# Optimization experiments

Measured on AMD Instinct MI355X. Metric: run time of the kernel, lower is better.

## Reference

```python
import jax, jax.numpy as jnp
import numpy as np

B, N, DIM, H, DH = 8, 4096, 512, 8, 64
M = 266  # nb_features = int(dim_head * ln(dim_head)) = int(64*4.1589)
LN_EPS = 1e-5
K_EPS = 1e-4  # performer softmax_kernel epsilon


def _gaussian_orthogonal_matrix(m, d, rng):
    # performer_pytorch default: stacked QR blocks, rows scaled by chi(d) norms
    blocks = []
    n_full = m // d
    for _ in range(n_full):
        q, _ = np.linalg.qr(rng.standard_normal((d, d)))
        blocks.append(q.T)
    rem = m - n_full * d
    if rem > 0:
        q, _ = np.linalg.qr(rng.standard_normal((d, d)))
        blocks.append(q.T[:rem])
    proj = np.concatenate(blocks, axis=0)
    norms = np.linalg.norm(rng.standard_normal((m, d)), axis=1)
    return (proj * norms[:, None]).astype(np.float32)


def setup_inputs() -> dict:
    key = jax.random.key(0)
    ks = jax.random.split(key, 8)
    s_in = 1.0 / np.sqrt(DIM)
    s_ff = 1.0 / np.sqrt(4 * DIM)
    rng = np.random.default_rng(0)
    return {
        "x": jax.random.normal(ks[0], (B, N, DIM), jnp.float32),
        "w_q": jax.random.normal(ks[1], (DIM, DIM), jnp.float32) * s_in,
        "w_k": jax.random.normal(ks[2], (DIM, DIM), jnp.float32) * s_in,
        "w_v": jax.random.normal(ks[3], (DIM, DIM), jnp.float32) * s_in,
        "w_o": jax.random.normal(ks[4], (DIM, DIM), jnp.float32) * s_in,
        "b_o": jnp.zeros((DIM,), jnp.float32),
        "ln1_g": jnp.ones((DIM,), jnp.float32),
        "ln1_b": jnp.zeros((DIM,), jnp.float32),
        "ln2_g": jnp.ones((DIM,), jnp.float32),
        "ln2_b": jnp.zeros((DIM,), jnp.float32),
        "ff_w1": jax.random.normal(ks[5], (DIM, 4 * DIM), jnp.float32) * s_in,
        "ff_b1": jnp.zeros((4 * DIM,), jnp.float32),
        "ff_w2": jax.random.normal(ks[6], (4 * DIM, DIM), jnp.float32) * s_ff,
        "ff_b2": jnp.zeros((DIM,), jnp.float32),
        "projection": jnp.asarray(_gaussian_orthogonal_matrix(M, DH, rng)),
    }


def _layernorm(x, g, b):
    mu = jnp.mean(x, -1, keepdims=True)
    var = jnp.mean((x - mu) ** 2, -1, keepdims=True)
    return (x - mu) * jax.lax.rsqrt(var + LN_EPS) * g + b


def _softmax_kernel(data, proj, is_query):
    # FAVOR+ positive softmax-kernel features (performer_pytorch.softmax_kernel)
    dn = data.shape[-1] ** -0.25  # data_normalizer
    ratio = proj.shape[0] ** -0.5
    dd = jnp.einsum("bhnd,md->bhnm", data * dn, proj)
    diag = jnp.sum(data ** 2, -1, keepdims=True) * 0.5 * (dn ** 2)  # [B,H,N,1]
    if is_query:
        mx = jax.lax.stop_gradient(jnp.max(dd, -1, keepdims=True))
    else:
        mx = jax.lax.stop_gradient(jnp.max(dd))
    return ratio * (jnp.exp(dd - diag - mx) + K_EPS)


def reference(x, w_q, w_k, w_v, w_o, b_o, ln1_g, ln1_b, ln2_g, ln2_b,
              ff_w1, ff_b1, ff_w2, ff_b2, projection):
    # --- attention sublayer (pre-norm) ---
    h = _layernorm(x, ln1_g, ln1_b)

    def split_heads(t):
        return t.reshape(B, N, H, DH).transpose(0, 2, 1, 3)  # [B,H,N,DH]

    q = split_heads(h @ w_q)
    k = split_heads(h @ w_k)
    v = split_heads(h @ w_v)

    qp = _softmax_kernel(q, projection, True)   # [B,H,N,M]
    kp = _softmax_kernel(k, projection, False)  # [B,H,N,M]

    # non-causal linear attention: O(N) in sequence length
    d_inv = 1.0 / jnp.einsum("bhnm,bhm->bhn", qp, jnp.sum(kp, axis=2))
    ctx = jnp.einsum("bhnm,bhnd->bhmd", kp, v)          # [B,H,M,DH]
    attn = jnp.einsum("bhnm,bhmd,bhn->bhnd", qp, ctx, d_inv)
    attn = attn.transpose(0, 2, 1, 3).reshape(B, N, DIM)
    x = x + attn @ w_o + b_o

    # --- feed-forward sublayer (pre-norm) ---
    h2 = _layernorm(x, ln2_g, ln2_b)
    ff = jax.nn.gelu(h2 @ ff_w1 + ff_b1, approximate=False) @ ff_w2 + ff_b2
    return x + ff
```

## Files before the change

kernel.cpp:

```cpp
#include <hip/hip_runtime.h>
#include <cmath>

typedef unsigned short u16;
typedef unsigned int u32;
typedef short bf16x8 __attribute__((ext_vector_type(8)));
typedef float f32x4 __attribute__((ext_vector_type(4)));

#define DEVI __device__ __forceinline__

constexpr int NSEQ = 4096, DIMM = 512;
constexpr int KVLD = 1024;
constexpr int MP = 288;
constexpr int MPP = 296;
constexpr int MREAL = 266;
constexpr int DHP = 96;
constexpr int LSTR = 72;
constexpr float LNEPS = 1e-5f;
constexpr float KEPS = 1e-4f;
constexpr float DN = 0.3535533905932738f;
constexpr float HALF_DN2 = 0.0625f;

DEVI u16 f2bf(float f) {
  u32 u = __float_as_uint(f);
  u32 r = (u + 0x7FFFu + ((u >> 16) & 1u)) >> 16;
  return (u16)r;
}
DEVI float bf2f(u16 h) { return __uint_as_float(((u32)h) << 16); }

DEVI f32x4 mfma16(bf16x8 a, bf16x8 b, f32x4 c) {
  return __builtin_amdgcn_mfma_f32_16x16x32_bf16(a, b, c, 0, 0, 0);
}

DEVI void gload_lds16(const void* g, void* l) {
  __builtin_amdgcn_global_load_lds(
      (const __attribute__((address_space(1))) u32*)g,
      (__attribute__((address_space(3))) u32*)l, 16, 0, 0);
}

DEVI float gelu_fast(float z) {
  float a = fminf(1.5957691216057308f * (z + 0.044715f * z * z * z), 60.f);
  float e = __expf(a);
  return z * e * __builtin_amdgcn_rcpf(e + 1.f);
}

__global__ void ws_sentinel(float* out) { out[0] = 12345.0f; }

__launch_bounds__(256)
__global__ void transpose_cvt(const float* __restrict__ in, u16* __restrict__ out,
                              int K, int Nn) {
  __shared__ float tl[32][33];
  int ntn = Nn >> 5;
  int bid = blockIdx.x;
  int kt = bid / ntn, ntt = bid - kt * ntn;
  int k0 = kt << 5, nn0 = ntt << 5;
  int t = threadIdx.x;
  int r = t >> 5, c = t & 31;
#pragma unroll
  for (int i = 0; i < 4; ++i)
    tl[r + i * 8][c] = in[(size_t)(k0 + r + i * 8) * Nn + nn0 + c];
  __syncthreads();
#pragma unroll
  for (int i = 0; i < 4; ++i)
    out[(size_t)(nn0 + r + i * 8) * K + k0 + c] = f2bf(tl[c][r + i * 8]);
}

__global__ void proj_prep(const float* __restrict__ proj, u16* __restrict__ projf) {
  int idx = blockIdx.x * 256 + threadIdx.x;
  if (idx >= MP * 64) return;
  int e = idx & 7, lane = (idx >> 3) & 63, fh = idx >> 9;
  int f = fh >> 1, half = fh & 1;
  int m = f * 16 + (lane & 15);
  int d = half * 32 + (lane >> 4) * 8 + e;
  float v = (m < MREAL) ? proj[m * 64 + d] * DN : 0.f;
  projf[idx] = f2bf(v);
}

__launch_bounds__(256)
__global__ void ln_fwd(const float* __restrict__ x, const float* __restrict__ g,
                       const float* __restrict__ bt, u16* __restrict__ out) {
  int w = threadIdx.x >> 6, lane = threadIdx.x & 63;
  int row = blockIdx.x * 4 + w;
  const float* xr = x + (size_t)row * DIMM;
  int c0 = lane * 4;
  float4 v0 = *(const float4*)(xr + c0);
  float4 v1 = *(const float4*)(xr + 256 + c0);
  float s = v0.x + v0.y + v0.z + v0.w + v1.x + v1.y + v1.z + v1.w;
  float sq = v0.x * v0.x + v0.y * v0.y + v0.z * v0.z + v0.w * v0.w +
             v1.x * v1.x + v1.y * v1.y + v1.z * v1.z + v1.w * v1.w;
#pragma unroll
  for (int mk = 1; mk < 64; mk <<= 1) {
    s += __shfl_xor(s, mk, 64);
    sq += __shfl_xor(sq, mk, 64);
  }
  float mu = s * (1.f / 512.f);
  float var = sq * (1.f / 512.f) - mu * mu;
  float rstd = rsqrtf(var + LNEPS);
  float4 g0 = *(const float4*)(g + c0);
  float4 g1 = *(const float4*)(g + 256 + c0);
  float4 b0 = *(const float4*)(bt + c0);
  float4 b1 = *(const float4*)(bt + 256 + c0);
  u16* orow = out + (size_t)row * DIMM;
  uint2 p0, p1;
  {
    u16 h0 = f2bf((v0.x - mu) * rstd * g0.x + b0.x);
    u16 h1 = f2bf((v0.y - mu) * rstd * g0.y + b0.y);
    u16 h2 = f2bf((v0.z - mu) * rstd * g0.z + b0.z);
    u16 h3 = f2bf((v0.w - mu) * rstd * g0.w + b0.w);
    p0.x = ((u32)h1 << 16) | h0; p0.y = ((u32)h3 << 16) | h2;
  }
  {
    u16 h0 = f2bf((v1.x - mu) * rstd * g1.x + b1.x);
    u16 h1 = f2bf((v1.y - mu) * rstd * g1.y + b1.y);
    u16 h2 = f2bf((v1.z - mu) * rstd * g1.z + b1.z);
    u16 h3 = f2bf((v1.w - mu) * rstd * g1.w + b1.w);
    p1.x = ((u32)h1 << 16) | h0; p1.y = ((u32)h3 << 16) | h2;
  }
  *(uint2*)(orow + c0) = p0;
  *(uint2*)(orow + 256 + c0) = p1;
}

#define WAITVM(N) asm volatile("s_waitcnt vmcnt(" #N ")" ::: "memory")

template <int EPI>
__launch_bounds__(512)
__global__ void gemm256(const u16* __restrict__ A, int lda,
                        const u16* __restrict__ Bt, int ldb, int K,
                        void* __restrict__ OutP, int Nout, int ldo,
                        const float* __restrict__ bias,
                        const float* __restrict__ Res) {
  __shared__ __align__(16) u16 Al[2][256 * 64];
  __shared__ __align__(16) u16 Bl[2][256 * 64];
  int ntiles = Nout >> 8;
  int nwg = gridDim.x;
  int bid = blockIdx.x;
  int cpx = nwg >> 3;
  int wg = (bid & 7) * cpx + (bid >> 3);
  int mt = wg / ntiles, nt = wg - mt * ntiles;
  int t = threadIdx.x, lane = t & 63, w = t >> 6;
  int wm = w >> 2, wn = w & 3;
  int fr = lane & 15, fq = lane >> 4;
  int rowA0 = mt * 256, colB0 = nt * 256;
  int swz = (fr & 7) << 4;

  f32x4 acc[8][4];
#pragma unroll
  for (int i = 0; i < 8; ++i)
#pragma unroll
    for (int j = 0; j < 4; ++j) acc[i][j] = f32x4{0.f, 0.f, 0.f, 0.f};

  int srow = t >> 3;
  int so = ((t * 16) & 127) ^ ((srow & 7) << 4);

#define STAGE_G(bufi, k0)                                                       \
  do {                                                                          \
    _Pragma("unroll") for (int it = 0; it < 4; ++it) {                          \
      gload_lds16(                                                              \
          (const char*)(A + ((size_t)(rowA0 + srow + it * 64) * lda + (k0))) + so, \
          (char*)Al[bufi] + t * 16 + it * 8192);                                \
      gload_lds16(                                                              \
          (const char*)(Bt + ((size_t)(colB0 + srow + it * 64) * ldb + (k0))) + so, \
          (char*)Bl[bufi] + t * 16 + it * 8192);                                \
    }                                                                           \
  } while (0)

  int NT = K >> 6;
  STAGE_G(0, 0);
  STAGE_G(1, 64);
  int bi = 0;
  for (int tt = 0; tt < NT; ++tt) {
    if (tt + 1 < NT) { WAITVM(8); } else { WAITVM(0); }
    __builtin_amdgcn_s_barrier();
#pragma unroll
    for (int p = 0; p < 4; ++p) {
      int mh = p >> 1, nh = p & 1;
      bf16x8 av[4][2], bv[2][2];
#pragma unroll
      for (int i = 0; i < 4; ++i)
#pragma unroll
        for (int ks = 0; ks < 2; ++ks) {
          int row = wm * 128 + (mh * 4 + i) * 16 + fr;
          av[i][ks] = *(const bf16x8*)((const char*)Al[bi] + row * 128 +
                                       (((ks << 6) | (fq << 4)) ^ swz));
        }
#pragma unroll
      for (int j = 0; j < 2; ++j)
#pragma unroll
        for (int ks = 0; ks < 2; ++ks) {
          int row = wn * 64 + (nh * 2 + j) * 16 + fr;
          bv[j][ks] = *(const bf16x8*)((const char*)Bl[bi] + row * 128 +
                                       (((ks << 6) | (fq << 4)) ^ swz));
        }
      __builtin_amdgcn_s_setprio(1);
#pragma unroll
      for (int i = 0; i < 4; ++i)
#pragma unroll
        for (int j = 0; j < 2; ++j)
#pragma unroll
          for (int ks = 0; ks < 2; ++ks)
            acc[mh * 4 + i][nh * 2 + j] =
                mfma16(av[i][ks], bv[j][ks], acc[mh * 4 + i][nh * 2 + j]);
      __builtin_amdgcn_s_setprio(0);
    }
    __builtin_amdgcn_s_barrier();
    if (tt + 2 < NT) STAGE_G(bi, (tt + 2) * 64);
    bi ^= 1;
  }
#undef STAGE_G

#pragma unroll
  for (int i = 0; i < 8; ++i)
#pragma unroll
    for (int j = 0; j < 4; ++j) {
      int row = rowA0 + wm * 128 + i * 16 + fq * 4;
      int col = colB0 + wn * 64 + j * 16 + fr;
#pragma unroll
      for (int r = 0; r < 4; ++r) {
        float v = acc[i][j][r];
        size_t idx = (size_t)(row + r) * ldo + col;
        if constexpr (EPI == 0) {
          ((u16*)OutP)[idx] = f2bf(v);
        } else if constexpr (EPI == 1) {
          ((float*)OutP)[idx] = v + bias[col] + Res[(size_t)(row + r) * 512 + col];
        } else if constexpr (EPI == 2) {
          ((u16*)OutP)[idx] = f2bf(gelu_fast(v + bias[col]));
        } else {
          float bb = bias ? bias[col] : 0.f;
          ((float*)OutP)[idx] += v + bb;
        }
      }
    }
}

__launch_bounds__(256)
__global__ void kmax_kernel(const u16* __restrict__ kv, const u16* __restrict__ projf,
                            u32* __restrict__ maxslot) {
  __shared__ __align__(16) u16 kt[64 * 64];
  __shared__ float wred[4];
  int bid = blockIdx.x;
  int bh = bid >> 6, nt = bid & 63;
  int b = bh >> 3, h = bh & 7;
  int n0 = nt * 64;
  int t = threadIdx.x, lane = t & 63, w = t >> 6;
  int fr = lane & 15, fq = lane >> 4;

#pragma unroll
  for (int it = 0; it < 4; ++it) {
    int idx = t + it * 256;
    int r = idx >> 4, sg = idx & 15;
    *(uint2*)(kt + r * 64 + sg * 4) =
        *(const uint2*)(kv + ((size_t)(b * NSEQ + n0 + r)) * KVLD + h * 64 + sg * 4);
  }
  __syncthreads();

  const bf16x8* pf = (const bf16x8*)projf;
  bf16x8 a0 = *(const bf16x8*)(kt + (w * 16 + fr) * 64 + fq * 8);
  bf16x8 a1 = *(const bf16x8*)(kt + (w * 16 + fr) * 64 + 32 + fq * 8);
  float m = -1e30f;
#pragma unroll
  for (int f = 0; f < 18; ++f) {
    bf16x8 b0 = pf[(f * 2 + 0) * 64 + lane];
    bf16x8 b1 = pf[(f * 2 + 1) * 64 + lane];
    f32x4 z = {0.f, 0.f, 0.f, 0.f};
    z = mfma16(a0, b0, z);
    z = mfma16(a1, b1, z);
    if (f * 16 + fr < MREAL) {
#pragma unroll
      for (int r = 0; r < 4; ++r) m = fmaxf(m, z[r]);
    }
  }
#pragma unroll
  for (int mk = 1; mk < 64; mk <<= 1) m = fmaxf(m, __shfl_xor(m, mk, 64));
  if (lane == 0) wred[w] = m;
  __syncthreads();
  if (t == 0) {
    float mm = fmaxf(fmaxf(wred[0], wred[1]), fmaxf(wred[2], wred[3]));
    u32 u = __float_as_uint(mm);
    u32 enc = (u & 0x80000000u) ? ~u : (u | 0x80000000u);
    atomicMax(maxslot, enc);
  }
}

__launch_bounds__(512)
__global__ void fused_ctx(const u16* __restrict__ kvbuf, const u16* __restrict__ projf,
                          const u32* __restrict__ maxslot, float* __restrict__ part) {
  __shared__ __align__(16) u16 kt[64 * 64];
  __shared__ __align__(16) u16 kpL[MP * LSTR];
  __shared__ __align__(16) u16 vL[DHP * LSTR];
  int bid = blockIdx.x;
  int bh = bid >> 2, s = bid & 3;
  int b = bh >> 3, h = bh & 7;
  int t = threadIdx.x, lane = t & 63, w = t >> 6;
  int fr = lane & 15, fq = lane >> 4;
  int rg = w & 3, fh = w >> 2;
  int wq4 = w >> 1, wn = w & 1;
  int i_base = (wq4 < 2) ? wq4 * 5 : 10 + (wq4 - 2) * 4;
  int i_cnt = (wq4 < 2) ? 5 : 4;

  if (t < 256) {
    int rr = 64 + (t >> 3), sg = t & 7;
    u16 val = (rr == 64) ? (u16)0x3F80 : (u16)0;
    uint4 v4; u16* pv = (u16*)&v4;
#pragma unroll
    for (int e = 0; e < 8; ++e) pv[e] = val;
    *(uint4*)(vL + rr * LSTR + sg * 8) = v4;
  }
  u32 enc = *maxslot;
  float gmax = __uint_as_float((enc & 0x80000000u) ? (enc & 0x7FFFFFFFu) : ~enc);
  const bf16x8* pf = (const bf16x8*)projf;

  f32x4 acc[5][3];
#pragma unroll
  for (int i = 0; i < 5; ++i)
#pragma unroll
    for (int j = 0; j < 3; ++j) acc[i][j] = f32x4{0.f, 0.f, 0.f, 0.f};

  for (int tile = 0; tile < 16; ++tile) {
    int n0 = s * 1024 + tile * 64;
#pragma unroll
    for (int it = 0; it < 2; ++it) {
      int idx = t + it * 512;
      int r = idx >> 4, sg = idx & 15;
      *(uint2*)(kt + r * 64 + sg * 4) =
          *(const uint2*)(kvbuf + ((size_t)(b * NSEQ + n0 + r)) * KVLD + h * 64 + sg * 4);
    }
#pragma unroll
    for (int it = 0; it < 2; ++it) {
      int idx = t + it * 512;
      int r = idx >> 4, sg = idx & 15;
      uint2 val = *(const uint2*)(kvbuf + ((size_t)(b * NSEQ + n0 + r)) * KVLD + 512 + h * 64 + sg * 4);
      u16* pv = (u16*)&val;
#pragma unroll
      for (int e = 0; e < 4; ++e) vL[(sg * 4 + e) * LSTR + r] = pv[e];
    }
    __syncthreads();

    float dg[4];
#pragma unroll
    for (int r4 = 0; r4 < 4; ++r4) {
      int row = rg * 16 + fq * 4 + r4;
      const u16* kr = kt + row * 64 + fr * 4;
      float ssum = 0.f;
#pragma unroll
      for (int e = 0; e < 4; ++e) { float xv = bf2f(kr[e]); ssum += xv * xv; }
#pragma unroll
      for (int mk = 1; mk < 16; mk <<= 1) ssum += __shfl_xor(ssum, mk, 64);
      dg[r4] = ssum * HALF_DN2;
    }
    bf16x8 a0 = *(const bf16x8*)(kt + (rg * 16 + fr) * 64 + fq * 8);
    bf16x8 a1 = *(const bf16x8*)(kt + (rg * 16 + fr) * 64 + 32 + fq * 8);
#pragma unroll
    for (int ff = 0; ff < 9; ++ff) {
      int f = fh * 9 + ff;
      bf16x8 b0 = pf[(f * 2 + 0) * 64 + lane];
      bf16x8 b1 = pf[(f * 2 + 1) * 64 + lane];
      f32x4 z = {0.f, 0.f, 0.f, 0.f};
      z = mfma16(a0, b0, z);
      z = mfma16(a1, b1, z);
      int col = f * 16 + fr;
#pragma unroll
      for (int r4 = 0; r4 < 4; ++r4) {
        int row = rg * 16 + fq * 4 + r4;
        float kval = (col < MREAL) ? (__expf(z[r4] - dg[r4] - gmax) + KEPS) : 0.f;
        kpL[col * LSTR + row] = f2bf(kval);
      }
    }
    __syncthreads();

#pragma unroll
    for (int kc = 0; kc < 2; ++kc) {
      bf16x8 av[5], bv[3];
#pragma unroll
      for (int i = 0; i < 5; ++i)
        if (i < i_cnt)
          av[i] = *(const bf16x8*)(kpL + ((i_base + i) * 16 + fr) * LSTR + kc * 32 + fq * 8);
#pragma unroll
      for (int j = 0; j < 3; ++j)
        bv[j] = *(const bf16x8*)(vL + (wn * 48 + j * 16 + fr) * LSTR + kc * 32 + fq * 8);
#pragma unroll
      for (int i = 0; i < 5; ++i)
        if (i < i_cnt)
#pragma unroll
          for (int j = 0; j < 3; ++j) acc[i][j] = mfma16(av[i], bv[j], acc[i][j]);
    }
    __syncthreads();
  }

  float* dst = part + ((size_t)bh * 4 + s) * MP * DHP;
#pragma unroll
  for (int i = 0; i < 5; ++i)
    if (i < i_cnt)
#pragma unroll
      for (int j = 0; j < 3; ++j) {
        int m = (i_base + i) * 16 + fq * 4;
        int c = wn * 48 + j * 16 + fr;
#pragma unroll
        for (int r = 0; r < 4; ++r) dst[(size_t)(m + r) * DHP + c] = acc[i][j][r];
      }
}

__launch_bounds__(256)
__global__ void ctx_reduce2(const float* __restrict__ part, u16* __restrict__ ctxT) {
  int bh = blockIdx.x, t = threadIdx.x;
  const float* p = part + (size_t)bh * 4 * MP * DHP;
  u16* dst = ctxT + (size_t)bh * DHP * MP;
  for (int idx = t; idx < DHP * MP; idx += 256) {
    int d = idx / MP, m = idx - d * MP;
    size_t o = (size_t)m * DHP + d;
    float v = p[o] + p[o + MP * DHP] + p[o + 2 * MP * DHP] + p[o + 3 * MP * DHP];
    dst[idx] = f2bf(v);
  }
}

__launch_bounds__(256)
__global__ void fused_attn(const u16* __restrict__ qb, const u16* __restrict__ ctxT,
                           const u16* __restrict__ projf, u16* __restrict__ attnb) {
  __shared__ __align__(16) u16 qt[64 * 64];
  __shared__ __align__(16) u16 qpL[64 * MPP];
  __shared__ float dbuf[64];
  int bid = blockIdx.x;
  int bh = bid >> 6, nt = bid & 63;
  int b = bh >> 3, h = bh & 7;
  int n0 = nt * 64;
  int t = threadIdx.x, lane = t & 63, w = t >> 6;
  int wm = w >> 1, wn = w & 1;
  int fr = lane & 15, fq = lane >> 4;

#pragma unroll
  for (int it = 0; it < 4; ++it) {
    int idx = t + it * 256;
    int r = idx >> 4, sg = idx & 15;
    *(uint2*)(qt + r * 64 + sg * 4) =
        *(const uint2*)(qb + ((size_t)(b * NSEQ + n0 + r)) * KVLD + h * 64 + sg * 4);
  }
  __syncthreads();

  float dg[4];
#pragma unroll
  for (int r4 = 0; r4 < 4; ++r4) {
    int row = w * 16 + fq * 4 + r4;
    const u16* qr = qt + row * 64 + fr * 4;
    float ssum = 0.f;
#pragma unroll
    for (int e = 0; e < 4; ++e) { float xv = bf2f(qr[e]); ssum += xv * xv; }
#pragma unroll
    for (int mk = 1; mk < 16; mk <<= 1) ssum += __shfl_xor(ssum, mk, 64);
    dg[r4] = ssum * HALF_DN2;
  }
  const bf16x8* pf = (const bf16x8*)projf;
  bf16x8 a0 = *(const bf16x8*)(qt + (w * 16 + fr) * 64 + fq * 8);
  bf16x8 a1 = *(const bf16x8*)(qt + (w * 16 + fr) * 64 + 32 + fq * 8);
  f32x4 accf[18];
#pragma unroll
  for (int f = 0; f < 18; ++f) {
    bf16x8 b0 = pf[(f * 2 + 0) * 64 + lane];
    bf16x8 b1 = pf[(f * 2 + 1) * 64 + lane];
    f32x4 z = {0.f, 0.f, 0.f, 0.f};
    z = mfma16(a0, b0, z);
    z = mfma16(a1, b1, z);
    accf[f] = z;
  }
  float mx[4];
#pragma unroll
  for (int r4 = 0; r4 < 4; ++r4) {
    float mm = -1e30f;
#pragma unroll
    for (int f = 0; f < 18; ++f) mm = fmaxf(mm, accf[f][r4]);
#pragma unroll
    for (int mk = 1; mk < 16; mk <<= 1) mm = fmaxf(mm, __shfl_xor(mm, mk, 64));
    mx[r4] = mm;
  }
#pragma unroll
  for (int f = 0; f < 18; ++f) {
    int col = f * 16 + fr;
#pragma unroll
    for (int r4 = 0; r4 < 4; ++r4) {
      int row = w * 16 + fq * 4 + r4;
      float qv = __expf(accf[f][r4] - dg[r4] - mx[r4]) + KEPS;
      qpL[row * MPP + col] = f2bf(qv);
    }
  }
  __syncthreads();

  const u16* cg = ctxT + (size_t)bh * DHP * MP;
  f32x4 acc2[2][3];
#pragma unroll
  for (int i = 0; i < 2; ++i)
#pragma unroll
    for (int j = 0; j < 3; ++j) acc2[i][j] = f32x4{0.f, 0.f, 0.f, 0.f};
  for (int k0 = 0; k0 < MP; k0 += 32) {
    bf16x8 av[2], bv[3];
#pragma unroll
    for (int i = 0; i < 2; ++i)
      av[i] = *(const bf16x8*)(qpL + (wm * 32 + i * 16 + fr) * MPP + k0 + fq * 8);
#pragma unroll
    for (int j = 0; j < 3; ++j)
      bv[j] = *(const bf16x8*)(cg + (size_t)(wn * 48 + j * 16 + fr) * MP + k0 + fq * 8);
#pragma unroll
    for (int i = 0; i < 2; ++i)
#pragma unroll
      for (int j = 0; j < 3; ++j) acc2[i][j] = mfma16(av[i], bv[j], acc2[i][j]);
  }
  if (wn == 1 && fr == 0) {
#pragma unroll
    for (int i = 0; i < 2; ++i) {
      int rl = wm * 32 + i * 16 + fq * 4;
#pragma unroll
      for (int r = 0; r < 4; ++r) dbuf[rl + r] = acc2[i][1][r];
    }
  }
  __syncthreads();

  u16* ob = qt;
#pragma unroll
  for (int i = 0; i < 2; ++i)
#pragma unroll
    for (int j = 0; j < 3; ++j) {
      int cl = wn * 48 + j * 16 + fr;
      if (cl < 64) {
        int rl = wm * 32 + i * 16 + fq * 4;
#pragma unroll
        for (int r = 0; r < 4; ++r)
          ob[(rl + r) * 64 + cl] = f2bf(acc2[i][j][r] / dbuf[rl + r]);
      }
    }
  __syncthreads();

  u16* dst = attnb + ((size_t)(b * NSEQ + n0)) * KVLD + h * 64;
  for (int idx = t; idx < 64 * 8; idx += 256) {
    int r = idx >> 3, sg = idx & 7;
    *(uint4*)(dst + (size_t)r * KVLD + sg * 8) = *(const uint4*)(ob + r * 64 + sg * 8);
  }
}

constexpr size_t OFF_WQT   = 0;
constexpr size_t OFF_WKT   = 524288;
constexpr size_t OFF_WVT   = 1048576;
constexpr size_t OFF_WOT   = 1572864;
constexpr size_t OFF_FF1T  = 2097152;
constexpr size_t OFF_FF2T  = 4194304;
constexpr size_t OFF_PROJF = 6328320;
constexpr size_t OFF_MAX   = 6365184;
constexpr size_t OFF_CTXT  = 6365440;
constexpr size_t OFF_H     = 9904384;
constexpr size_t OFF_KV    = 43458816;
constexpr size_t OFF_PART  = 110567680;
constexpr size_t WS_NEED   = 138879232;

extern "C" void kernel_launch(void* const* d_in, const int* in_sizes, int n_in,
                              void* d_out, int out_size, void* d_ws, size_t ws_size,
                              hipStream_t stream) {
  const float* x    = (const float*)d_in[0];
  const float* w_q  = (const float*)d_in[1];
  const float* w_k  = (const float*)d_in[2];
  const float* w_v  = (const float*)d_in[3];
  const float* w_o  = (const float*)d_in[4];
  const float* b_o  = (const float*)d_in[5];
  const float* ln1g = (const float*)d_in[6];
  const float* ln1b = (const float*)d_in[7];
  const float* ln2g = (const float*)d_in[8];
  const float* ln2b = (const float*)d_in[9];
  const float* ffw1 = (const float*)d_in[10];
  const float* ffb1 = (const float*)d_in[11];
  const float* ffw2 = (const float*)d_in[12];
  const float* ffb2 = (const float*)d_in[13];
  const float* proj = (const float*)d_in[14];
  (void)in_sizes; (void)n_in; (void)out_size;

  float* dout = (float*)d_out;
  if (ws_size < WS_NEED) {
    ws_sentinel<<<1, 1, 0, stream>>>(dout);
    return;
  }

  char* ws = (char*)d_ws;
  u16* wqt   = (u16*)(ws + OFF_WQT);
  u16* wkt   = (u16*)(ws + OFF_WKT);
  u16* wvt   = (u16*)(ws + OFF_WVT);
  u16* wot   = (u16*)(ws + OFF_WOT);
  u16* ff1t  = (u16*)(ws + OFF_FF1T);
  u16* ff2t  = (u16*)(ws + OFF_FF2T);
  u16* projf = (u16*)(ws + OFF_PROJF);
  u32* maxsl = (u32*)(ws + OFF_MAX);
  u16* ctxt  = (u16*)(ws + OFF_CTXT);
  u16* hbuf  = (u16*)(ws + OFF_H);
  u16* kvbuf = (u16*)(ws + OFF_KV);
  float* part = (float*)(ws + OFF_PART);

  hipMemsetAsync(maxsl, 0, 4, stream);

  transpose_cvt<<<256, 256, 0, stream>>>(w_q, wqt, 512, 512);
  transpose_cvt<<<256, 256, 0, stream>>>(w_k, wkt, 512, 512);
  transpose_cvt<<<256, 256, 0, stream>>>(w_v, wvt, 512, 512);
  transpose_cvt<<<256, 256, 0, stream>>>(w_o, wot, 512, 512);
  transpose_cvt<<<1024, 256, 0, stream>>>(ffw1, ff1t, 512, 2048);
  transpose_cvt<<<1024, 256, 0, stream>>>(ffw2, ff2t, 2048, 512);
  proj_prep<<<72, 256, 0, stream>>>(proj, projf);

  ln_fwd<<<8192, 256, 0, stream>>>(x, ln1g, ln1b, hbuf);
  gemm256<0><<<512, 512, 0, stream>>>(hbuf, 512, wkt, 512, 512, kvbuf, 1024, 1024, nullptr, nullptr);
  kmax_kernel<<<4096, 256, 0, stream>>>(kvbuf, projf, maxsl);
  fused_ctx<<<256, 512, 0, stream>>>(kvbuf, projf, maxsl, part);
  ctx_reduce2<<<64, 256, 0, stream>>>(part, ctxt);
  gemm256<0><<<256, 512, 0, stream>>>(hbuf, 512, wqt, 512, 512, kvbuf, 512, 1024, nullptr, nullptr);
  fused_attn<<<4096, 256, 0, stream>>>(kvbuf, ctxt, projf, kvbuf + 512);
  gemm256<1><<<256, 512, 0, stream>>>(kvbuf + 512, 1024, wot, 512, 512, dout, 512, 512, b_o, x);
  ln_fwd<<<8192, 256, 0, stream>>>(dout, ln2g, ln2b, hbuf);
  for (int c = 0; c < 2; ++c) {
    gemm256<2><<<512, 512, 0, stream>>>(hbuf, 512, ff1t + (size_t)c * 1024 * 512, 512, 512,
                                        kvbuf, 1024, 1024, ffb1 + c * 1024, nullptr);
    gemm256<3><<<256, 512, 0, stream>>>(kvbuf, 1024, ff2t + c * 1024, 2048, 1024,
                                        dout, 512, 512, (c == 0) ? ffb2 : nullptr, nullptr);
  }
}
```

Baseline: 665.5 us.

## Make attention feature kernels warp-local, loading Q/K fragments directly from global

Both kmax_kernel and fused_attn now load their MFMA A-fragments straight from global memory instead of staging the Q/K tile through shared memory with a block barrier. In fused_attn the MFMA operands are swapped so each lane's outputs belong to a single row, which turns the diagonal and max reductions into two cross-lane shuffles. Each wave then handles its own 16 rows end to end through per-wave shared buffers, so every __syncthreads is removed. Features are packed with v_cvt_pk_bf16_f32 and written as 8-byte stores. In exchange, each wave now computes all 80 ctx columns itself, and the ctx reads from global are no longer shared between waves.

```diff
diff --git a/kernel.cpp b/kernel.cpp
--- a/kernel.cpp
+++ b/kernel.cpp
@@ -234,7 +234,6 @@
 __launch_bounds__(256)
 __global__ void kmax_kernel(const u16* __restrict__ kv, const u16* __restrict__ projf,
                             u32* __restrict__ maxslot) {
-  __shared__ __align__(16) u16 kt[64 * 64];
   __shared__ float wred[4];
   int bid = blockIdx.x;
   int bh = bid >> 6, nt = bid & 63;
@@ -243,18 +242,11 @@
   int t = threadIdx.x, lane = t & 63, w = t >> 6;
   int fr = lane & 15, fq = lane >> 4;
 
-#pragma unroll
-  for (int it = 0; it < 4; ++it) {
-    int idx = t + it * 256;
-    int r = idx >> 4, sg = idx & 15;
-    *(uint2*)(kt + r * 64 + sg * 4) =
-        *(const uint2*)(kv + ((size_t)(b * NSEQ + n0 + r)) * KVLD + h * 64 + sg * 4);
-  }
-  __syncthreads();
+  const u16* krow = kv + ((size_t)(b * NSEQ + n0 + w * 16 + fr)) * KVLD + h * 64;
+  bf16x8 a0 = *(const bf16x8*)(krow + fq * 8);
+  bf16x8 a1 = *(const bf16x8*)(krow + 32 + fq * 8);
 
   const bf16x8* pf = (const bf16x8*)projf;
-  bf16x8 a0 = *(const bf16x8*)(kt + (w * 16 + fr) * 64 + fq * 8);
-  bf16x8 a1 = *(const bf16x8*)(kt + (w * 16 + fr) * 64 + 32 + fq * 8);
   float m = -1e30f;
 #pragma unroll
   for (int f = 0; f < 18; ++f) {
@@ -414,121 +406,86 @@
 __launch_bounds__(256)
 __global__ void fused_attn(const u16* __restrict__ qb, const u16* __restrict__ ctxT,
                            const u16* __restrict__ projf, u16* __restrict__ attnb) {
-  __shared__ __align__(16) u16 qt[64 * 64];
-  __shared__ __align__(16) u16 qpL[64 * MPP];
-  __shared__ float dbuf[64];
+  __shared__ __align__(16) u16 qpW[4][16 * MPP];
+  __shared__ __align__(16) u16 obW[4][16 * 64];
   int bid = blockIdx.x;
   int bh = bid >> 6, nt = bid & 63;
   int b = bh >> 3, h = bh & 7;
   int n0 = nt * 64;
   int t = threadIdx.x, lane = t & 63, w = t >> 6;
-  int wm = w >> 1, wn = w & 1;
   int fr = lane & 15, fq = lane >> 4;
 
-#pragma unroll
-  for (int it = 0; it < 4; ++it) {
-    int idx = t + it * 256;
-    int r = idx >> 4, sg = idx & 15;
-    *(uint2*)(qt + r * 64 + sg * 4) =
-        *(const uint2*)(qb + ((size_t)(b * NSEQ + n0 + r)) * KVLD + h * 64 + sg * 4);
-  }
-  __syncthreads();
-
-  float dg[4];
-#pragma unroll
-  for (int r4 = 0; r4 < 4; ++r4) {
-    int row = w * 16 + fq * 4 + r4;
-    const u16* qr = qt + row * 64 + fr * 4;
-    float ssum = 0.f;
-#pragma unroll
-    for (int e = 0; e < 4; ++e) { float xv = bf2f(qr[e]); ssum += xv * xv; }
-#pragma unroll
-    for (int mk = 1; mk < 16; mk <<= 1) ssum += __shfl_xor(ssum, mk, 64);
-    dg[r4] = ssum * HALF_DN2;
-  }
+  const u16* qrow = qb + ((size_t)(b * NSEQ + n0 + w * 16 + fr)) * KVLD + h * 64;
+  bf16x8 a0 = *(const bf16x8*)(qrow + fq * 8);
+  bf16x8 a1 = *(const bf16x8*)(qrow + 32 + fq * 8);
+
+  float ss = 0.f;
+#pragma unroll
+  for (int e = 0; e < 8; ++e) {
+    float x0 = bf2f((u16)a0[e]), x1 = bf2f((u16)a1[e]);
+    ss += x0 * x0 + x1 * x1;
+  }
+  ss += __shfl_xor(ss, 16, 64);
+  ss += __shfl_xor(ss, 32, 64);
+  float dg = ss * HALF_DN2;
+
   const bf16x8* pf = (const bf16x8*)projf;
-  bf16x8 a0 = *(const bf16x8*)(qt + (w * 16 + fr) * 64 + fq * 8);
-  bf16x8 a1 = *(const bf16x8*)(qt + (w * 16 + fr) * 64 + 32 + fq * 8);
   f32x4 accf[18];
 #pragma unroll
   for (int f = 0; f < 18; ++f) {
-    bf16x8 b0 = pf[(f * 2 + 0) * 64 + lane];
-    bf16x8 b1 = pf[(f * 2 + 1) * 64 + lane];
     f32x4 z = {0.f, 0.f, 0.f, 0.f};
-    z = mfma16(a0, b0, z);
-    z = mfma16(a1, b1, z);
+    z = mfma16(pf[(f * 2 + 0) * 64 + lane], a0, z);
+    z = mfma16(pf[(f * 2 + 1) * 64 + lane], a1, z);
     accf[f] = z;
   }
-  float mx[4];
-#pragma unroll
-  for (int r4 = 0; r4 < 4; ++r4) {
-    float mm = -1e30f;
-#pragma unroll
-    for (int f = 0; f < 18; ++f) mm = fmaxf(mm, accf[f][r4]);
-#pragma unroll
-    for (int mk = 1; mk < 16; mk <<= 1) mm = fmaxf(mm, __shfl_xor(mm, mk, 64));
-    mx[r4] = mm;
-  }
+  float mm = -1e30f;
+#pragma unroll
+  for (int f = 0; f < 18; ++f)
+#pragma unroll
+    for (int r = 0; r < 4; ++r) mm = fmaxf(mm, accf[f][r]);
+  mm = fmaxf(mm, __shfl_xor(mm, 16, 64));
+  mm = fmaxf(mm, __shfl_xor(mm, 32, 64));
+
+  u16* qp = qpW[w] + fr * MPP + fq * 4;
 #pragma unroll
   for (int f = 0; f < 18; ++f) {
-    int col = f * 16 + fr;
-#pragma unroll
-    for (int r4 = 0; r4 < 4; ++r4) {
-      int row = w * 16 + fq * 4 + r4;
-      float qv = __expf(accf[f][r4] - dg[r4] - mx[r4]) + KEPS;
-      qpL[row * MPP + col] = f2bf(qv);
-    }
-  }
-  __syncthreads();
+    float e0 = __expf(accf[f][0] - dg - mm) + KEPS;
+    float e1 = __expf(accf[f][1] - dg - mm) + KEPS;
+    float e2 = __expf(accf[f][2] - dg - mm) + KEPS;
+    float e3 = __expf(accf[f][3] - dg - mm) + KEPS;
+    u32 lo, hi;
+    asm("v_cvt_pk_bf16_f32 %0, %1, %2" : "=v"(lo) : "v"(e0), "v"(e1));
+    asm("v_cvt_pk_bf16_f32 %0, %1, %2" : "=v"(hi) : "v"(e2), "v"(e3));
+    uint2 pk; pk.x = lo; pk.y = hi;
+    *(uint2*)(qp + f * 16) = pk;
+  }
 
   const u16* cg = ctxT + (size_t)bh * DHP * MP;
-  f32x4 acc2[2][3];
-#pragma unroll
-  for (int i = 0; i < 2; ++i)
-#pragma unroll
-    for (int j = 0; j < 3; ++j) acc2[i][j] = f32x4{0.f, 0.f, 0.f, 0.f};
-  for (int k0 = 0; k0 < MP; k0 += 32) {
-    bf16x8 av[2], bv[3];
-#pragma unroll
-    for (int i = 0; i < 2; ++i)
-      av[i] = *(const bf16x8*)(qpL + (wm * 32 + i * 16 + fr) * MPP + k0 + fq * 8);
-#pragma unroll
-    for (int j = 0; j < 3; ++j)
-      bv[j] = *(const bf16x8*)(cg + (size_t)(wn * 48 + j * 16 + fr) * MP + k0 + fq * 8);
-#pragma unroll
-    for (int i = 0; i < 2; ++i)
-#pragma unroll
-      for (int j = 0; j < 3; ++j) acc2[i][j] = mfma16(av[i], bv[j], acc2[i][j]);
-  }
-  if (wn == 1 && fr == 0) {
-#pragma unroll
-    for (int i = 0; i < 2; ++i) {
-      int rl = wm * 32 + i * 16 + fq * 4;
-#pragma unroll
-      for (int r = 0; r < 4; ++r) dbuf[rl + r] = acc2[i][1][r];
-    }
-  }
-  __syncthreads();
-
-  u16* ob = qt;
-#pragma unroll
-  for (int i = 0; i < 2; ++i)
-#pragma unroll
-    for (int j = 0; j < 3; ++j) {
-      int cl = wn * 48 + j * 16 + fr;
-      if (cl < 64) {
-        int rl = wm * 32 + i * 16 + fq * 4;
-#pragma unroll
-        for (int r = 0; r < 4; ++r)
-          ob[(rl + r) * 64 + cl] = f2bf(acc2[i][j][r] / dbuf[rl + r]);
-      }
-    }
-  __syncthreads();
-
-  u16* dst = attnb + ((size_t)(b * NSEQ + n0)) * KVLD + h * 64;
-  for (int idx = t; idx < 64 * 8; idx += 256) {
-    int r = idx >> 3, sg = idx & 7;
-    *(uint4*)(dst + (size_t)r * KVLD + sg * 8) = *(const uint4*)(ob + r * 64 + sg * 8);
+  f32x4 acc2[5];
+#pragma unroll
+  for (int j = 0; j < 5; ++j) acc2[j] = f32x4{0.f, 0.f, 0.f, 0.f};
+#pragma unroll
+  for (int kc = 0; kc < 9; ++kc) {
+    bf16x8 av = *(const bf16x8*)(qpW[w] + fr * MPP + kc * 32 + fq * 8);
+#pragma unroll
+    for (int j = 0; j < 5; ++j) {
+      bf16x8 bv = *(const bf16x8*)(cg + (size_t)(j * 16 + fr) * MP + kc * 32 + fq * 8);
+      acc2[j] = mfma16(av, bv, acc2[j]);
+    }
+  }
+  float dv[4];
+#pragma unroll
+  for (int r = 0; r < 4; ++r) dv[r] = __shfl(acc2[4][r], lane & 48, 64);
+#pragma unroll
+  for (int j = 0; j < 4; ++j)
+#pragma unroll
+    for (int r = 0; r < 4; ++r)
+      obW[w][(fq * 4 + r) * 64 + j * 16 + fr] = f2bf(acc2[j][r] / dv[r]);
+#pragma unroll
+  for (int it = 0; it < 2; ++it) {
+    int r = (lane >> 3) + it * 8, sg = lane & 7;
+    *(uint4*)(attnb + ((size_t)(b * NSEQ + n0 + w * 16 + r)) * KVLD + h * 64 + sg * 8) =
+        *(const uint4*)(obW[w] + r * 64 + sg * 8);
   }
 }
 
```

Result: slower. 715.7 us (+7.5%).

## Overlap next-tile global staging with second-half MFMAs; load K fragments directly in kmax

Applied to the files above, without the earlier changes.

The GEMM main loop now reads all A and B fragments for a k-tile into registers at once. It issues the first half of the MFMAs, waits for the LDS reads, passes the barrier and starts the next global-to-LDS stage, then issues the remaining MFMAs. This is meant to hide the staging latency behind compute, at the cost of many more live fragment registers, which can reduce occupancy or cause spills. Separately, kmax_kernel drops its LDS staging and __syncthreads and loads the MFMA operand fragments straight from global memory.

```diff
diff --git a/kernel.cpp b/kernel.cpp
--- a/kernel.cpp
+++ b/kernel.cpp
@@ -170,39 +170,49 @@
   for (int tt = 0; tt < NT; ++tt) {
     if (tt + 1 < NT) { WAITVM(8); } else { WAITVM(0); }
     __builtin_amdgcn_s_barrier();
-#pragma unroll
-    for (int p = 0; p < 4; ++p) {
-      int mh = p >> 1, nh = p & 1;
-      bf16x8 av[4][2], bv[2][2];
-#pragma unroll
-      for (int i = 0; i < 4; ++i)
-#pragma unroll
-        for (int ks = 0; ks < 2; ++ks) {
-          int row = wm * 128 + (mh * 4 + i) * 16 + fr;
-          av[i][ks] = *(const bf16x8*)((const char*)Al[bi] + row * 128 +
-                                       (((ks << 6) | (fq << 4)) ^ swz));
-        }
-#pragma unroll
-      for (int j = 0; j < 2; ++j)
-#pragma unroll
-        for (int ks = 0; ks < 2; ++ks) {
-          int row = wn * 64 + (nh * 2 + j) * 16 + fr;
-          bv[j][ks] = *(const bf16x8*)((const char*)Bl[bi] + row * 128 +
-                                       (((ks << 6) | (fq << 4)) ^ swz));
-        }
-      __builtin_amdgcn_s_setprio(1);
-#pragma unroll
-      for (int i = 0; i < 4; ++i)
-#pragma unroll
-        for (int j = 0; j < 2; ++j)
-#pragma unroll
-          for (int ks = 0; ks < 2; ++ks)
-            acc[mh * 4 + i][nh * 2 + j] =
-                mfma16(av[i][ks], bv[j][ks], acc[mh * 4 + i][nh * 2 + j]);
-      __builtin_amdgcn_s_setprio(0);
-    }
+
+    bf16x8 av[8][2], bv[4][2];
+#pragma unroll
+    for (int i = 0; i < 8; ++i)
+#pragma unroll
+      for (int ks = 0; ks < 2; ++ks) {
+        int row = wm * 128 + i * 16 + fr;
+        av[i][ks] = *(const bf16x8*)((const char*)Al[bi] + row * 128 +
+                                     (((ks << 6) | (fq << 4)) ^ swz));
+      }
+#pragma unroll
+    for (int j = 0; j < 4; ++j)
+#pragma unroll
+      for (int ks = 0; ks < 2; ++ks) {
+        int row = wn * 64 + (j)*16 + fr;
+        bv[j][ks] = *(const bf16x8*)((const char*)Bl[bi] + row * 128 +
+                                     (((ks << 6) | (fq << 4)) ^ swz));
+      }
+
+    __builtin_amdgcn_s_setprio(1);
+#pragma unroll
+    for (int i = 0; i < 4; ++i)
+#pragma unroll
+      for (int j = 0; j < 4; ++j)
+#pragma unroll
+        for (int ks = 0; ks < 2; ++ks)
+          acc[i][j] = mfma16(av[i][ks], bv[j][ks], acc[i][j]);
+    __builtin_amdgcn_s_setprio(0);
+
+    asm volatile("s_waitcnt lgkmcnt(0)" ::: "memory");
+    __builtin_amdgcn_sched_barrier(0);
     __builtin_amdgcn_s_barrier();
     if (tt + 2 < NT) STAGE_G(bi, (tt + 2) * 64);
+
+    __builtin_amdgcn_s_setprio(1);
+#pragma unroll
+    for (int i = 4; i < 8; ++i)
+#pragma unroll
+      for (int j = 0; j < 4; ++j)
+#pragma unroll
+        for (int ks = 0; ks < 2; ++ks)
+          acc[i][j] = mfma16(av[i][ks], bv[j][ks], acc[i][j]);
+    __builtin_amdgcn_s_setprio(0);
     bi ^= 1;
   }
 #undef STAGE_G
@@ -234,7 +244,6 @@
 __launch_bounds__(256)
 __global__ void kmax_kernel(const u16* __restrict__ kv, const u16* __restrict__ projf,
                             u32* __restrict__ maxslot) {
-  __shared__ __align__(16) u16 kt[64 * 64];
   __shared__ float wred[4];
   int bid = blockIdx.x;
   int bh = bid >> 6, nt = bid & 63;
@@ -243,18 +252,11 @@
   int t = threadIdx.x, lane = t & 63, w = t >> 6;
   int fr = lane & 15, fq = lane >> 4;
 
-#pragma unroll
-  for (int it = 0; it < 4; ++it) {
-    int idx = t + it * 256;
-    int r = idx >> 4, sg = idx & 15;
-    *(uint2*)(kt + r * 64 + sg * 4) =
-        *(const uint2*)(kv + ((size_t)(b * NSEQ + n0 + r)) * KVLD + h * 64 + sg * 4);
-  }
-  __syncthreads();
+  const u16* krow = kv + ((size_t)(b * NSEQ + n0 + w * 16 + fr)) * KVLD + h * 64;
+  bf16x8 a0 = *(const bf16x8*)(krow + fq * 8);
+  bf16x8 a1 = *(const bf16x8*)(krow + 32 + fq * 8);
 
   const bf16x8* pf = (const bf16x8*)projf;
-  bf16x8 a0 = *(const bf16x8*)(kt + (w * 16 + fr) * 64 + fq * 8);
-  bf16x8 a1 = *(const bf16x8*)(kt + (w * 16 + fr) * 64 + 32 + fq * 8);
   float m = -1e30f;
 #pragma unroll
   for (int f = 0; f < 18; ++f) {
```

Measured after the change: 630.0 us. 5.3% less time.
